# Optimization experiments

Hardware: AMD Instinct MI355X
Metric: run time of the kernel (lower is better)

The kernel has to match this reference:

```python
import jax, jax.numpy as jnp
import numpy as np

D_MODEL, D_INNER, D_STATE, DT_RANK, K = 768, 1536, 16, 48, 4
B, L = 2, 1024


def causal_depthwise_conv(x, w, b):
    # x: [B, L, D], w: [D, 1, K], b: [D]; torch pads K-1 both sides then slices [:L] -> causal left pad
    xt = x.transpose(0, 2, 1)  # [B, D, L]
    out = jax.lax.conv_general_dilated(
        xt, w, window_strides=(1,), padding=[(K - 1, 0)],
        dimension_numbers=('NCH', 'OIH', 'NCH'), feature_group_count=xt.shape[1])
    return out.transpose(0, 2, 1) + b


def ssm(xc, A_log, D, W_dt, dtW, dtb, W_B, W_C):
    # xc: [B, L, Din]
    A = -jnp.exp(A_log)                                   # [Din, N]
    dt_low = jnp.einsum('bld,rd->blr', xc, W_dt)          # [B, L, R]
    delta = jax.nn.softplus(jnp.einsum('blr,dr->bld', dt_low, dtW) + dtb)  # [B, L, Din]
    Bm = jnp.einsum('bld,nd->bln', xc, W_B)               # [B, L, N]
    Cm = jnp.einsum('bld,nd->bln', xc, W_C)               # [B, L, N]
    deltaA = jnp.exp(delta[..., None] * A)                # [B, L, Din, N]
    BX = (delta * xc)[..., None] * Bm[:, :, None, :]      # [B, L, Din, N]

    def combine(e1, e2):
        a1, b1 = e1
        a2, b2 = e2
        return a1 * a2, a2 * b1 + b2

    _, hs = jax.lax.associative_scan(combine, (deltaA, BX), axis=1)  # [B, L, Din, N]
    y = jnp.einsum('bldn,bln->bld', hs, Cm) + D * xc
    return y


def setup_inputs() -> dict:
    key = jax.random.key(0)
    ks = jax.random.split(key, 20)
    s = 0.02
    A_init = jnp.log(jnp.broadcast_to(jnp.arange(1, D_STATE + 1, dtype=jnp.float32), (D_INNER, D_STATE)))
    return {
        'x': jax.random.normal(ks[0], (B, L, D_MODEL), jnp.float32),
        'W_in_states': jax.random.normal(ks[1], (D_INNER, D_MODEL), jnp.float32) * s,
        'W_in_gates': jax.random.normal(ks[2], (D_INNER, D_MODEL), jnp.float32) * s,
        'conv_w': jax.random.normal(ks[3], (D_INNER, 1, K), jnp.float32) * 0.2,
        'conv_b': jax.random.normal(ks[4], (D_INNER,), jnp.float32) * 0.02,
        'conv_w_b': jax.random.normal(ks[5], (D_INNER, 1, K), jnp.float32) * 0.2,
        'conv_b_b': jax.random.normal(ks[6], (D_INNER,), jnp.float32) * 0.02,
        'W_dt': jax.random.normal(ks[7], (DT_RANK, D_INNER), jnp.float32) * s,
        'W_B': jax.random.normal(ks[8], (D_STATE, D_INNER), jnp.float32) * s,
        'W_C': jax.random.normal(ks[9], (D_STATE, D_INNER), jnp.float32) * s,
        'dtW': jax.random.normal(ks[10], (D_INNER, DT_RANK), jnp.float32) * s,
        'dtb': jax.random.normal(ks[11], (D_INNER,), jnp.float32) * 0.1,
        'A_log': A_init,
        'Dp': jnp.ones((D_INNER,), jnp.float32),
        'W_dt_b': jax.random.normal(ks[12], (DT_RANK, D_INNER), jnp.float32) * s,
        'W_B_b': jax.random.normal(ks[13], (D_STATE, D_INNER), jnp.float32) * s,
        'W_C_b': jax.random.normal(ks[14], (D_STATE, D_INNER), jnp.float32) * s,
        'dtW_b': jax.random.normal(ks[15], (D_INNER, DT_RANK), jnp.float32) * s,
        'dtb_b': jax.random.normal(ks[16], (D_INNER,), jnp.float32) * 0.1,
        'A_log_b': A_init,
        'Dp_b': jnp.ones((D_INNER,), jnp.float32),
        'W_out': jax.random.normal(ks[17], (D_MODEL, D_INNER), jnp.float32) * s,
    }


def reference(x, W_in_states, W_in_gates, conv_w, conv_b, conv_w_b, conv_b_b,
              W_dt, W_B, W_C, dtW, dtb, A_log, Dp,
              W_dt_b, W_B_b, W_C_b, dtW_b, dtb_b, A_log_b, Dp_b, W_out):
    xs = jnp.einsum('blm,dm->bld', x, W_in_states)  # [B, L, Din]
    z = jnp.einsum('blm,dm->bld', x, W_in_gates)    # [B, L, Din]
    # forward branch
    xc = jax.nn.silu(causal_depthwise_conv(xs, conv_w, conv_b))
    y = ssm(xc, A_log, Dp, W_dt, dtW, dtb, W_B, W_C)
    # backward branch: xz flipped along L, split -> reversed xs / reversed z
    xs_b = xs[:, ::-1]
    z_b = z[:, ::-1]
    xcb = jax.nn.silu(causal_depthwise_conv(xs_b, conv_w_b, conv_b_b))
    y_b = ssm(xcb, A_log_b, Dp_b, W_dt_b, dtW_b, dtb_b, W_B_b, W_C_b)
    # gating
    y = y * jax.nn.silu(z)
    y_b = y_b * jax.nn.silu(z_b)
    y = (y + y_b[:, ::-1]) * 0.5  # divide_output
    return jnp.einsum('bld,md->blm', y, W_out)
```

## Files before the change

### kernel.cpp

```cpp
#include <hip/hip_runtime.h>
#include <hip/hip_bf16.h>
#include <stdint.h>

#define DM 768
#define DI 1536
#define DSTATE 16
#define RNK 48
#define BB 2
#define LL 1024
#define ML (BB * LL)

#define NSEG 32
#define SEGL (LL / NSEG)

#define PROJ_NCHUNK 8
#define PROJ_KC (DI / PROJ_NCHUNK)

typedef unsigned short u16;
typedef __bf16 bf16x8 __attribute__((ext_vector_type(8)));
typedef float f32x4 __attribute__((ext_vector_type(4)));

struct __align__(8) u16x4_t { u16 x, y, z, w; };

__device__ __forceinline__ float b2f(u16 u) {
  union { uint32_t i; float f; } v; v.i = ((uint32_t)u) << 16; return v.f;
}
__device__ __forceinline__ u16 f2b(float f) {
  union { float f; uint32_t i; } v; v.f = f;
  uint32_t r = v.i + 0x7FFFu + ((v.i >> 16) & 1u);
  return (u16)(r >> 16);
}
__device__ __forceinline__ float silu_f(float x) { return x / (1.f + __expf(-x)); }
__device__ __forceinline__ float softplus_f(float s) {
  return fmaxf(s, 0.f) + __logf(1.f + __expf(-fabsf(s)));
}
__device__ __forceinline__ u16x4_t cvt4(float4 v) {
  u16x4_t o; o.x = f2b(v.x); o.y = f2b(v.y); o.z = f2b(v.z); o.w = f2b(v.w); return o;
}

__device__ __forceinline__ void gl16(const u16* g, u16* l) {
  __builtin_amdgcn_global_load_lds(
      (const __attribute__((address_space(1))) uint32_t*)g,
      (__attribute__((address_space(3))) uint32_t*)l, 16, 0, 0);
}

#define SEG_X    (ML * DM / 4)
#define SEG_W    (DI * DM / 4)
#define SEG_CAT  (128 * DI / 4)
#define SEG_DTW  (DI * 64 / 4)
__global__ __launch_bounds__(256) void convert_kernel(
    const float4* __restrict__ x, const float4* __restrict__ wis,
    const float4* __restrict__ wig, const float4* __restrict__ wout,
    const float* __restrict__ W_B, const float* __restrict__ W_C,
    const float* __restrict__ W_dt,
    const float* __restrict__ W_B_b, const float* __restrict__ W_C_b,
    const float* __restrict__ W_dt_b,
    const float* __restrict__ dtW, const float* __restrict__ dtW_b,
    u16x4_t* __restrict__ xb, u16x4_t* __restrict__ wisb,
    u16x4_t* __restrict__ wigb, u16x4_t* __restrict__ woutb,
    u16x4_t* __restrict__ wcf, u16x4_t* __restrict__ wcb,
    u16x4_t* __restrict__ dtwf, u16x4_t* __restrict__ dtwb)
{
  int idx = blockIdx.x * 256 + threadIdx.x;
  if (idx < SEG_X) { xb[idx] = cvt4(x[idx]); return; }
  idx -= SEG_X;
  if (idx < SEG_W) { wisb[idx] = cvt4(wis[idx]); return; }
  idx -= SEG_W;
  if (idx < SEG_W) { wigb[idx] = cvt4(wig[idx]); return; }
  idx -= SEG_W;
  if (idx < SEG_W) { woutb[idx] = cvt4(wout[idx]); return; }
  idx -= SEG_W;
  if (idx < 2 * SEG_CAT) {
    int dir = idx / SEG_CAT;
    int rem = idx % SEG_CAT;
    int row = rem / (DI / 4), k4 = rem % (DI / 4);
    const float* src = nullptr;
    if (row < 16)      src = (dir ? W_B_b  : W_B)  + (size_t)row * DI + k4 * 4;
    else if (row < 32) src = (dir ? W_C_b  : W_C)  + (size_t)(row - 16) * DI + k4 * 4;
    else if (row < 80) src = (dir ? W_dt_b : W_dt) + (size_t)(row - 32) * DI + k4 * 4;
    u16x4_t o;
    if (src) o = cvt4(*(const float4*)src);
    else { o.x = 0; o.y = 0; o.z = 0; o.w = 0; }
    (dir ? wcb : wcf)[rem] = o;
    return;
  }
  idx -= 2 * SEG_CAT;
  int dir = idx / SEG_DTW;
  int rem = idx % SEG_DTW;
  int d = rem / 16, r4 = rem % 16;
  const float* Dw = dir ? dtW_b : dtW;
  u16x4_t o;
  if (r4 < 12) o = cvt4(*(const float4*)(Dw + (size_t)d * RNK + r4 * 4));
  else { o.x = 0; o.y = 0; o.z = 0; o.w = 0; }
  (dir ? dtwb : dtwf)[rem] = o;
}

__global__ __launch_bounds__(256) void gemm_bt(
    const u16* __restrict__ A, const u16* __restrict__ B0,
    const u16* __restrict__ B1, int Nsplit,
    void* __restrict__ Cout, int M, int N, int K, int ldc, int epi)
{
  __shared__ alignas(16) u16 As[2][64 * 32];
  __shared__ alignas(16) u16 Bs[2][128 * 32];
  const int tid = threadIdx.x;
  const int wave = tid >> 6, lane = tid & 63;
  const int bm = blockIdx.y * 64;
  const int bn = blockIdx.x * 128;

  const u16* Bmat = B0;
  int ncol0 = bn;
  int epi_l = epi;
  if (B1 != nullptr && bn >= Nsplit) { Bmat = B1; ncol0 = bn - Nsplit; epi_l = 1; }

  const int c0 = tid, c1 = tid + 256;
  const u16* gA0 = A + (size_t)(bm + (c0 >> 2)) * K + (c0 & 3) * 8;
  const u16* gB0 = Bmat + (size_t)(ncol0 + (c0 >> 2)) * K + (c0 & 3) * 8;
  const u16* gB1 = Bmat + (size_t)(ncol0 + (c1 >> 2)) * K + (c1 & 3) * 8;

  const int wm = (wave & 1) * 32, wn = (wave >> 1) * 64;
  const int rl = lane & 15, q = lane >> 4;

  f32x4 acc[2][4];
#pragma unroll
  for (int i = 0; i < 2; ++i)
#pragma unroll
    for (int j = 0; j < 4; ++j) acc[i][j] = (f32x4){0.f, 0.f, 0.f, 0.f};

  auto stage = [&](int buf, int k0) {
    gl16(gA0 + k0, &As[buf][c0 * 8]);
    gl16(gB0 + k0, &Bs[buf][c0 * 8]);
    gl16(gB1 + k0, &Bs[buf][c1 * 8]);
  };

  stage(0, 0);
  __syncthreads();
  int cur = 0;
  for (int k0 = 0; k0 < K; k0 += 32) {
    const bool more = (k0 + 32 < K);
    if (more) stage(cur ^ 1, k0 + 32);

    const bf16x8* AsV = (const bf16x8*)As[cur];
    const bf16x8* BsV = (const bf16x8*)Bs[cur];
    bf16x8 af[2], bfv[4];
#pragma unroll
    for (int s = 0; s < 2; ++s)
      af[s] = AsV[(wm + s * 16 + rl) * 4 + q];
#pragma unroll
    for (int j = 0; j < 4; ++j)
      bfv[j] = BsV[(wn + j * 16 + rl) * 4 + q];
#pragma unroll
    for (int i = 0; i < 2; ++i)
#pragma unroll
      for (int j = 0; j < 4; ++j)
        acc[i][j] = __builtin_amdgcn_mfma_f32_16x16x32_bf16(af[i], bfv[j], acc[i][j], 0, 0, 0);

    if (more) {
      __syncthreads();
      cur ^= 1;
    }
  }

#pragma unroll
  for (int i = 0; i < 2; ++i) {
#pragma unroll
    for (int j = 0; j < 4; ++j) {
#pragma unroll
      for (int r = 0; r < 4; ++r) {
        int row = bm + wm + i * 16 + q * 4 + r;
        int col = bn + wn + j * 16 + rl;
        float v = acc[i][j][r];
        if (epi_l == 1) v = silu_f(v);
        ((u16*)Cout)[(size_t)row * ldc + col] = f2b(v);
      }
    }
  }
}

__global__ __launch_bounds__(256) void gemm_proj_sk(
    const u16* __restrict__ xcf, const u16* __restrict__ xcb,
    const u16* __restrict__ wcf, const u16* __restrict__ wcb,
    float* __restrict__ part)
{
  const int dir = blockIdx.z;
  const u16* A = dir ? xcb : xcf;
  const u16* B = dir ? wcb : wcf;
  const int kc = blockIdx.x;
  const int bm = blockIdx.y * 128;
  const int kbase = kc * PROJ_KC;

  __shared__ alignas(16) u16 As[128 * 32];
  __shared__ alignas(16) u16 Bs[128 * 32];
  const int tid = threadIdx.x;
  const int wave = tid >> 6, lane = tid & 63;
  const int c0 = tid, c1 = tid + 256;
  const u16* gA0 = A + (size_t)(bm + (c0 >> 2)) * DI + kbase + (c0 & 3) * 8;
  const u16* gA1 = A + (size_t)(bm + (c1 >> 2)) * DI + kbase + (c1 & 3) * 8;
  const u16* gB0 = B + (size_t)(c0 >> 2) * DI + kbase + (c0 & 3) * 8;
  const u16* gB1 = B + (size_t)(c1 >> 2) * DI + kbase + (c1 & 3) * 8;
  uint4* lA0 = (uint4*)&As[c0 * 8]; uint4* lA1 = (uint4*)&As[c1 * 8];
  uint4* lB0 = (uint4*)&Bs[c0 * 8]; uint4* lB1 = (uint4*)&Bs[c1 * 8];

  const int wm = (wave & 1) * 64, wn = (wave >> 1) * 64;
  const int rl = lane & 15, q = lane >> 4;

  f32x4 acc[4][4];
#pragma unroll
  for (int i = 0; i < 4; ++i)
#pragma unroll
    for (int j = 0; j < 4; ++j) acc[i][j] = (f32x4){0.f, 0.f, 0.f, 0.f};

  const bf16x8* AsV = (const bf16x8*)As;
  const bf16x8* BsV = (const bf16x8*)Bs;

  uint4 ra0 = *(const uint4*)(gA0);
  uint4 ra1 = *(const uint4*)(gA1);
  uint4 rb0 = *(const uint4*)(gB0);
  uint4 rb1 = *(const uint4*)(gB1);

  for (int k0 = 0; k0 < PROJ_KC; k0 += 32) {
    *lA0 = ra0; *lA1 = ra1; *lB0 = rb0; *lB1 = rb1;
    __syncthreads();
    if (k0 + 32 < PROJ_KC) {
      ra0 = *(const uint4*)(gA0 + k0 + 32);
      ra1 = *(const uint4*)(gA1 + k0 + 32);
      rb0 = *(const uint4*)(gB0 + k0 + 32);
      rb1 = *(const uint4*)(gB1 + k0 + 32);
    }
    bf16x8 af[4], bfv[4];
#pragma unroll
    for (int s = 0; s < 4; ++s) {
      af[s]  = AsV[(wm + s * 16 + rl) * 4 + q];
      bfv[s] = BsV[(wn + s * 16 + rl) * 4 + q];
    }
#pragma unroll
    for (int i = 0; i < 4; ++i)
#pragma unroll
      for (int j = 0; j < 4; ++j)
        acc[i][j] = __builtin_amdgcn_mfma_f32_16x16x32_bf16(af[i], bfv[j], acc[i][j], 0, 0, 0);
    __syncthreads();
  }

  float* pout = part + ((size_t)(dir * PROJ_NCHUNK + kc) * ML + bm) * 128;
#pragma unroll
  for (int i = 0; i < 4; ++i) {
#pragma unroll
    for (int j = 0; j < 4; ++j) {
#pragma unroll
      for (int r = 0; r < 4; ++r) {
        int row = wm + i * 16 + q * 4 + r;
        int col = wn + j * 16 + rl;
        if (col < 96)
          pout[(size_t)row * 128 + col] = acc[i][j][r];
      }
    }
  }
}

__global__ __launch_bounds__(256) void proj_reduce(
    const float* __restrict__ part,
    float* __restrict__ pf, float* __restrict__ pb,
    u16* __restrict__ dtlf, u16* __restrict__ dtlb)
{
  int idx = blockIdx.x * 256 + threadIdx.x;
  int col = idx % 96;
  int t = idx / 96;
  int row = t % ML;
  int dir = t / ML;
  const float* p = part + ((size_t)dir * PROJ_NCHUNK * ML + row) * 128 + col;
  float s = 0.f;
#pragma unroll
  for (int c = 0; c < PROJ_NCHUNK; ++c)
    s += p[(size_t)c * ML * 128];
  if (col < 32) (dir ? pb : pf)[(size_t)row * 32 + col] = s;
  else          (dir ? dtlb : dtlf)[(size_t)row * 64 + (col - 32)] = f2b(s);
}

__global__ __launch_bounds__(256) void gemm_delta(
    const u16* __restrict__ dtlf, const u16* __restrict__ dtlb,
    const u16* __restrict__ dtwf, const u16* __restrict__ dtwb,
    const float* __restrict__ dtb, const float* __restrict__ dtb_b,
    u16* __restrict__ df, u16* __restrict__ db)
{
  const int dir = blockIdx.z;
  const u16* A = dir ? dtlb : dtlf;
  const u16* Bw = dir ? dtwb : dtwf;
  const float* eb = dir ? dtb_b : dtb;
  u16* Cout = dir ? db : df;
  const int bm = blockIdx.y * 128;
  const int bn = blockIdx.x * 128;

  __shared__ alignas(16) u16 As[128 * 64];
  __shared__ alignas(16) u16 Bs[128 * 64];
  const int tid = threadIdx.x;
  const int wave = tid >> 6, lane = tid & 63;

#pragma unroll
  for (int i = 0; i < 4; ++i) {
    int c = tid + i * 256;
    gl16(A  + (size_t)(bm + (c >> 3)) * 64 + (c & 7) * 8, &As[c * 8]);
    gl16(Bw + (size_t)(bn + (c >> 3)) * 64 + (c & 7) * 8, &Bs[c * 8]);
  }
  __syncthreads();

  const int wm = (wave & 1) * 64, wn = (wave >> 1) * 64;
  const int rl = lane & 15, q = lane >> 4;

  f32x4 acc[4][4];
#pragma unroll
  for (int i = 0; i < 4; ++i)
#pragma unroll
    for (int j = 0; j < 4; ++j) acc[i][j] = (f32x4){0.f, 0.f, 0.f, 0.f};

#pragma unroll
  for (int kk = 0; kk < 2; ++kk) {
    bf16x8 af[4], bfv[4];
#pragma unroll
    for (int s = 0; s < 4; ++s) {
      af[s]  = *(const bf16x8*)&As[(wm + s * 16 + rl) * 64 + kk * 32 + q * 8];
      bfv[s] = *(const bf16x8*)&Bs[(wn + s * 16 + rl) * 64 + kk * 32 + q * 8];
    }
#pragma unroll
    for (int i = 0; i < 4; ++i)
#pragma unroll
      for (int j = 0; j < 4; ++j)
        acc[i][j] = __builtin_amdgcn_mfma_f32_16x16x32_bf16(af[i], bfv[j], acc[i][j], 0, 0, 0);
  }

#pragma unroll
  for (int i = 0; i < 4; ++i) {
#pragma unroll
    for (int j = 0; j < 4; ++j) {
#pragma unroll
      for (int r = 0; r < 4; ++r) {
        int row = bm + wm + i * 16 + q * 4 + r;
        int col = bn + wn + j * 16 + rl;
        Cout[(size_t)row * DI + col] = f2b(softplus_f(acc[i][j][r] + eb[col]));
      }
    }
  }
}

__global__ __launch_bounds__(256) void gemm_out64(
    const u16* __restrict__ A, const u16* __restrict__ Bw,
    float* __restrict__ out)
{
  __shared__ alignas(16) u16 As[64 * 72];
  __shared__ alignas(16) u16 Bs[64 * 72];
  const int tid = threadIdx.x;
  const int wave = tid >> 6, lane = tid & 63;
  const int bm = blockIdx.y * 64;
  const int bn = blockIdx.x * 64;

  const int c0 = tid, c1 = tid + 256;
  const u16* gA0 = A + (size_t)(bm + (c0 >> 3)) * DI + (c0 & 7) * 8;
  const u16* gA1 = A + (size_t)(bm + (c1 >> 3)) * DI + (c1 & 7) * 8;
  const u16* gB0 = Bw + (size_t)(bn + (c0 >> 3)) * DI + (c0 & 7) * 8;
  const u16* gB1 = Bw + (size_t)(bn + (c1 >> 3)) * DI + (c1 & 7) * 8;
  uint4* lA0 = (uint4*)&As[(c0 >> 3) * 72 + (c0 & 7) * 8];
  uint4* lA1 = (uint4*)&As[(c1 >> 3) * 72 + (c1 & 7) * 8];
  uint4* lB0 = (uint4*)&Bs[(c0 >> 3) * 72 + (c0 & 7) * 8];
  uint4* lB1 = (uint4*)&Bs[(c1 >> 3) * 72 + (c1 & 7) * 8];

  const int rl = lane & 15, q = lane >> 4;

  f32x4 acc[4];
#pragma unroll
  for (int s = 0; s < 4; ++s) acc[s] = (f32x4){0.f, 0.f, 0.f, 0.f};

  uint4 ra0 = *(const uint4*)gA0, ra1 = *(const uint4*)gA1;
  uint4 rb0 = *(const uint4*)gB0, rb1 = *(const uint4*)gB1;

  for (int k0 = 0; k0 < DI; k0 += 64) {
    *lA0 = ra0; *lA1 = ra1; *lB0 = rb0; *lB1 = rb1;
    __syncthreads();
    if (k0 + 64 < DI) {
      ra0 = *(const uint4*)(gA0 + k0 + 64);
      ra1 = *(const uint4*)(gA1 + k0 + 64);
      rb0 = *(const uint4*)(gB0 + k0 + 64);
      rb1 = *(const uint4*)(gB1 + k0 + 64);
    }
    bf16x8 bf[2], af;
#pragma unroll
    for (int c = 0; c < 2; ++c)
      bf[c] = *(const bf16x8*)&Bs[(wave * 16 + rl) * 72 + c * 32 + q * 8];
#pragma unroll
    for (int s = 0; s < 4; ++s) {
#pragma unroll
      for (int c = 0; c < 2; ++c) {
        af = *(const bf16x8*)&As[(s * 16 + rl) * 72 + c * 32 + q * 8];
        acc[s] = __builtin_amdgcn_mfma_f32_16x16x32_bf16(af, bf[c], acc[s], 0, 0, 0);
      }
    }
    __syncthreads();
  }

#pragma unroll
  for (int s = 0; s < 4; ++s) {
#pragma unroll
    for (int r = 0; r < 4; ++r) {
      int row = bm + s * 16 + q * 4 + r;
      int col = bn + wave * 16 + rl;
      out[(size_t)row * DM + col] = acc[s][r];
    }
  }
}

__global__ void conv_kernel(
    const u16* __restrict__ xsg,
    const float* __restrict__ cw, const float* __restrict__ cb,
    const float* __restrict__ cwb, const float* __restrict__ cbb,
    u16* __restrict__ xc, u16* __restrict__ xcb)
{
  int idx = blockIdx.x * 256 + threadIdx.x;
  int d = idx % DI;
  int row = idx / DI;
  int l = row % LL, b = row / LL;
  const u16* base = xsg + (size_t)b * LL * 3072 + d;

  float4 wf = *(const float4*)(cw + d * 4);
  float4 wb = *(const float4*)(cwb + d * 4);
  float wfk[4] = {wf.x, wf.y, wf.z, wf.w};
  float wbk[4] = {wb.x, wb.y, wb.z, wb.w};

  float accf = cb[d];
  float accb = cbb[d];
#pragma unroll
  for (int k = 0; k < 4; ++k) {
    int ls = l - 3 + k;
    if (ls >= 0) {
      accf += wfk[k] * b2f(base[(size_t)ls * 3072]);
      accb += wbk[k] * b2f(base[(size_t)(LL - 1 - ls) * 3072]);
    }
  }
  xc[idx]  = f2b(silu_f(accf));
  xcb[idx] = f2b(silu_f(accb));
}

__global__ __launch_bounds__(256) void scan_sum(
    const u16* __restrict__ df, const u16* __restrict__ db,
    const u16* __restrict__ xcf, const u16* __restrict__ xcb,
    const float* __restrict__ pf, const float* __restrict__ pb,
    const float* __restrict__ A_log, const float* __restrict__ A_log_b,
    float* __restrict__ sdl, float* __restrict__ bs)
{
  const int dir = blockIdx.z / NSEG, seg = blockIdx.z % NSEG;
  const u16* delta = dir ? db : df;
  const u16* xc = dir ? xcb : xcf;
  const float* proj = dir ? pb : pf;
  const float* Al = dir ? A_log_b : A_log;
  const int b = blockIdx.y;
  const int d = blockIdx.x * 256 + threadIdx.x;
  const int l0 = seg * SEGL;

  __shared__ float Bsh[SEGL][16];
  for (int i = threadIdx.x; i < SEGL * 16; i += 256) {
    int l = i >> 4, n = i & 15;
    Bsh[l][n] = proj[((size_t)b * LL + l0 + l) * 32 + n];
  }
  __syncthreads();

  float An[16];
#pragma unroll
  for (int n = 0; n < 16; ++n) An[n] = -__expf(Al[d * 16 + n]);

  float h[16];
#pragma unroll
  for (int n = 0; n < 16; ++n) h[n] = 0.f;
  float S = 0.f;

  const u16* dbase = delta + ((size_t)b * LL + l0) * DI + d;
  const u16* xbase = xc + ((size_t)b * LL + l0) * DI + d;

  for (int g = 0; g < SEGL; g += 4) {
    float dl4[4], dx4[4];
#pragma unroll
    for (int j = 0; j < 4; ++j) {
      float dv = b2f(dbase[(size_t)(g + j) * DI]);
      float xv = b2f(xbase[(size_t)(g + j) * DI]);
      dl4[j] = dv; dx4[j] = dv * xv;
    }
#pragma unroll
    for (int j = 0; j < 4; ++j) {
      S += dl4[j];
#pragma unroll
      for (int n = 0; n < 16; ++n)
        h[n] = __expf(dl4[j] * An[n]) * h[n] + dx4[j] * Bsh[g + j][n];
    }
  }

  size_t base = (((size_t)dir * BB + b) * NSEG + seg) * DI + d;
  sdl[base] = S;
#pragma unroll
  for (int n = 0; n < 16; ++n) bs[base * 16 + n] = h[n];
}

__global__ __launch_bounds__(256) void scan_carry(
    const float* __restrict__ A_log, const float* __restrict__ A_log_b,
    const float* __restrict__ sdl, float* __restrict__ bs)
{
  int idx = blockIdx.x * 256 + threadIdx.x;
  int n = idx & 15;
  int t = idx >> 4;
  int d = t % DI;
  int b = (t / DI) % BB;
  int dir = t / (DI * BB);
  const float* Al = dir ? A_log_b : A_log;
  float An = -__expf(Al[d * 16 + n]);
  float h = 0.f;
  for (int s = 0; s < NSEG; ++s) {
    size_t base = (((size_t)dir * BB + b) * NSEG + s) * DI + d;
    float S = sdl[base];
    float bv = bs[base * 16 + n];
    bs[base * 16 + n] = h;
    h = __expf(S * An) * h + bv;
  }
}

__global__ __launch_bounds__(512) void scan_apply2(
    const u16* __restrict__ df, const u16* __restrict__ db,
    const u16* __restrict__ xcf, const u16* __restrict__ xcb,
    const float* __restrict__ pf, const float* __restrict__ pb,
    const float* __restrict__ A_log, const float* __restrict__ A_log_b,
    const float* __restrict__ Dp, const float* __restrict__ Dp_b,
    const float* __restrict__ bs, const u16* __restrict__ xsg,
    u16* __restrict__ yc)
{
  const int s = blockIdx.z;
  const int b = blockIdx.y;
  const int tid = threadIdx.x;
  const int half = tid >> 8;
  const int td = tid & 255;
  const int d = blockIdx.x * 256 + td;

  __shared__ float BCsh[2][SEGL][32];
  __shared__ u16 ysh[2][SEGL][256];

  const int seg = half ? (NSEG - 1 - s) : s;
  const int l0 = seg * SEGL;
  const float* proj = half ? pb : pf;
  const float* Al   = half ? A_log_b : A_log;
  const float* Dpp  = half ? Dp_b : Dp;
  const u16* delta  = half ? db : df;
  const u16* xc     = half ? xcb : xcf;

  for (int i = td; i < SEGL * 32; i += 256) {
    int l = i >> 5, j = i & 31;
    BCsh[half][l][j] = proj[((size_t)b * LL + l0 + l) * 32 + j];
  }
  __syncthreads();

  float An[16];
#pragma unroll
  for (int n = 0; n < 16; ++n) An[n] = -__expf(Al[d * 16 + n]);
  const float Dv = Dpp[d];

  float h[16];
  size_t cbase = (((size_t)half * BB + b) * NSEG + seg) * DI + d;
#pragma unroll
  for (int n = 0; n < 16; ++n) h[n] = bs[cbase * 16 + n];

  const u16* dbase = delta + ((size_t)b * LL + l0) * DI + d;
  const u16* xbase = xc + ((size_t)b * LL + l0) * DI + d;

  for (int g = 0; g < SEGL; g += 4) {
    float dl4[4], xv4[4];
#pragma unroll
    for (int j = 0; j < 4; ++j) {
      dl4[j] = b2f(dbase[(size_t)(g + j) * DI]);
      xv4[j] = b2f(xbase[(size_t)(g + j) * DI]);
    }
#pragma unroll
    for (int j = 0; j < 4; ++j) {
      float dx = dl4[j] * xv4[j];
      float yv = 0.f;
#pragma unroll
      for (int n = 0; n < 16; ++n) {
        h[n] = __expf(dl4[j] * An[n]) * h[n] + dx * BCsh[half][g + j][n];
        yv += h[n] * BCsh[half][g + j][16 + n];
      }
      ysh[half][g + j][td] = f2b(yv + Dv * xv4[j]);
    }
  }
  __syncthreads();

  for (int i = tid; i < SEGL * 256; i += 512) {
    int lrow = i >> 8, dd = i & 255;
    int l = s * SEGL + lrow;
    int dg = blockIdx.x * 256 + dd;
    float gate = b2f(xsg[((size_t)b * LL + l) * 3072 + DI + dg]);
    float out = 0.5f * (b2f(ysh[0][lrow][dd]) +
                        b2f(ysh[1][SEGL - 1 - lrow][dd])) * gate;
    yc[((size_t)b * LL + l) * DI + dg] = f2b(out);
  }
}

extern "C" void kernel_launch(void* const* d_in, const int* in_sizes, int n_in,
                              void* d_out, int out_size, void* d_ws, size_t ws_size,
                              hipStream_t stream)
{
  const float* x       = (const float*)d_in[0];
  const float* Wis     = (const float*)d_in[1];
  const float* Wig     = (const float*)d_in[2];
  const float* conv_w  = (const float*)d_in[3];
  const float* conv_b  = (const float*)d_in[4];
  const float* conv_wb = (const float*)d_in[5];
  const float* conv_bb = (const float*)d_in[6];
  const float* W_dt    = (const float*)d_in[7];
  const float* W_B     = (const float*)d_in[8];
  const float* W_C     = (const float*)d_in[9];
  const float* dtW     = (const float*)d_in[10];
  const float* dtb     = (const float*)d_in[11];
  const float* A_log   = (const float*)d_in[12];
  const float* Dp      = (const float*)d_in[13];
  const float* W_dt_b  = (const float*)d_in[14];
  const float* W_B_b   = (const float*)d_in[15];
  const float* W_C_b   = (const float*)d_in[16];
  const float* dtW_b   = (const float*)d_in[17];
  const float* dtb_b   = (const float*)d_in[18];
  const float* A_log_b = (const float*)d_in[19];
  const float* Dp_b    = (const float*)d_in[20];
  const float* W_out   = (const float*)d_in[21];

  char* ws = (char*)d_ws;
  size_t off = 0;
  auto alloc = [&](size_t bytes) -> char* {
    char* p = ws + off; off += (bytes + 255) & ~(size_t)255; return p;
  };
  u16*   xb    = (u16*)alloc((size_t)ML * DM * 2);
  u16*   wisb  = (u16*)alloc((size_t)DI * DM * 2);
  u16*   wigb  = (u16*)alloc((size_t)DI * DM * 2);
  u16*   woutb = (u16*)alloc((size_t)DM * DI * 2);
  u16*   xsg = (u16*)alloc((size_t)ML * 3072 * 2);
  u16*   xc  = (u16*)alloc((size_t)ML * DI * 2);
  u16*   xcb = (u16*)alloc((size_t)ML * DI * 2);
  u16*   wcf = (u16*)alloc((size_t)128 * DI * 2);
  u16*   wcb = (u16*)alloc((size_t)128 * DI * 2);
  u16*   dtwf = (u16*)alloc((size_t)DI * 64 * 2);
  u16*   dtwb = (u16*)alloc((size_t)DI * 64 * 2);
  float* pf  = (float*)alloc((size_t)ML * 32 * 4);
  float* pb  = (float*)alloc((size_t)ML * 32 * 4);
  u16*   dtlf = (u16*)alloc((size_t)ML * 64 * 2);
  u16*   dtlb = (u16*)alloc((size_t)ML * 64 * 2);
  u16*   df  = (u16*)alloc((size_t)ML * DI * 2);
  u16*   db  = (u16*)alloc((size_t)ML * DI * 2);
  u16*   yc  = (u16*)alloc((size_t)ML * DI * 2);
  float* sdl = (float*)alloc((size_t)2 * BB * NSEG * DI * 4);
  float* bs  = (float*)alloc((size_t)2 * BB * NSEG * DI * 16 * 4);
  float* part = (float*)alloc((size_t)2 * PROJ_NCHUNK * ML * 128 * 4);

  const int conv_total = SEG_X + 3 * SEG_W + 2 * SEG_CAT + 2 * SEG_DTW;
  convert_kernel<<<(conv_total + 255) / 256, 256, 0, stream>>>(
      (const float4*)x, (const float4*)Wis, (const float4*)Wig, (const float4*)W_out,
      W_B, W_C, W_dt, W_B_b, W_C_b, W_dt_b, dtW, dtW_b,
      (u16x4_t*)xb, (u16x4_t*)wisb, (u16x4_t*)wigb, (u16x4_t*)woutb,
      (u16x4_t*)wcf, (u16x4_t*)wcb, (u16x4_t*)dtwf, (u16x4_t*)dtwb);

  gemm_bt<<<dim3(3072 / 128, ML / 64, 1), 256, 0, stream>>>(
      xb, wisb, wigb, DI, xsg, ML, 3072, DM, 3072, 0);

  conv_kernel<<<(ML * DI) / 256, 256, 0, stream>>>(
      xsg, conv_w, conv_b, conv_wb, conv_bb, xc, xcb);

  gemm_proj_sk<<<dim3(PROJ_NCHUNK, ML / 128, 2), 256, 0, stream>>>(
      xc, xcb, wcf, wcb, part);
  proj_reduce<<<(2 * ML * 96) / 256, 256, 0, stream>>>(
      part, pf, pb, dtlf, dtlb);

  gemm_delta<<<dim3(DI / 128, ML / 128, 2), 256, 0, stream>>>(
      dtlf, dtlb, dtwf, dtwb, dtb, dtb_b, df, db);

  scan_sum<<<dim3(DI / 256, BB, 2 * NSEG), 256, 0, stream>>>(
      df, db, xc, xcb, pf, pb, A_log, A_log_b, sdl, bs);
  scan_carry<<<(2 * BB * DI * 16) / 256, 256, 0, stream>>>(
      A_log, A_log_b, sdl, bs);
  scan_apply2<<<dim3(DI / 256, BB, NSEG), 512, 0, stream>>>(
      df, db, xc, xcb, pf, pb, A_log, A_log_b, Dp, Dp_b, bs, xsg, yc);

  gemm_out64<<<dim3(DM / 64, ML / 64, 1), 256, 0, stream>>>(
      yc, woutb, (float*)d_out);
}
```

Measured before the change: 256.4 us.

## Store delta and conv output channel-major so scans load contiguous time vectors

The delta GEMM swaps its operands so it writes delta in [D, B*L] layout, and the conv kernel now computes 8 consecutive timesteps per thread and also writes transposed copies of xc/xcb. The scan kernels then read 8 bf16 timesteps per 16-byte load instead of strided per-timestep scalar loads. This is meant to cut memory transactions in the scan phase. In exchange it adds extra transposed buffers and 16-byte-strided writes in conv, plus transposed stores in gemm_delta that may coalesce less well.

```diff
diff --git a/kernel.cpp b/kernel.cpp
--- a/kernel.cpp
+++ b/kernel.cpp
@@ -282,8 +282,8 @@
     u16* __restrict__ df, u16* __restrict__ db)
 {
   const int dir = blockIdx.z;
-  const u16* A = dir ? dtlb : dtlf;
-  const u16* Bw = dir ? dtwb : dtwf;
+  const u16* Aw = dir ? dtwb : dtwf;
+  const u16* Bl = dir ? dtlb : dtlf;
   const float* eb = dir ? dtb_b : dtb;
   u16* Cout = dir ? db : df;
   const int bm = blockIdx.y * 128;
@@ -297,8 +297,8 @@
 #pragma unroll
   for (int i = 0; i < 4; ++i) {
     int c = tid + i * 256;
-    gl16(A  + (size_t)(bm + (c >> 3)) * 64 + (c & 7) * 8, &As[c * 8]);
-    gl16(Bw + (size_t)(bn + (c >> 3)) * 64 + (c & 7) * 8, &Bs[c * 8]);
+    gl16(Aw + (size_t)(bm + (c >> 3)) * 64 + (c & 7) * 8, &As[c * 8]);
+    gl16(Bl + (size_t)(bn + (c >> 3)) * 64 + (c & 7) * 8, &Bs[c * 8]);
   }
   __syncthreads();
 
@@ -334,7 +334,7 @@
       for (int r = 0; r < 4; ++r) {
         int row = bm + wm + i * 16 + q * 4 + r;
         int col = bn + wn + j * 16 + rl;
-        Cout[(size_t)row * DI + col] = f2b(softplus_f(acc[i][j][r] + eb[col]));
+        Cout[(size_t)row * ML + col] = f2b(softplus_f(acc[i][j][r] + eb[row]));
       }
     }
   }
@@ -405,35 +405,53 @@
   }
 }
 
-__global__ void conv_kernel(
+__global__ __launch_bounds__(256) void conv_kernel(
     const u16* __restrict__ xsg,
     const float* __restrict__ cw, const float* __restrict__ cb,
     const float* __restrict__ cwb, const float* __restrict__ cbb,
-    u16* __restrict__ xc, u16* __restrict__ xcb)
-{
-  int idx = blockIdx.x * 256 + threadIdx.x;
-  int d = idx % DI;
-  int row = idx / DI;
-  int l = row % LL, b = row / LL;
+    u16* __restrict__ xc, u16* __restrict__ xcb,
+    u16* __restrict__ xct, u16* __restrict__ xcbt)
+{
+  int g = blockIdx.x * 256 + threadIdx.x;
+  int d = g % DI;
+  int lg = g / DI;
+  int b = lg >> 7;
+  int l0 = (lg & 127) * 8;
   const u16* base = xsg + (size_t)b * LL * 3072 + d;
 
   float4 wf = *(const float4*)(cw + d * 4);
   float4 wb = *(const float4*)(cwb + d * 4);
   float wfk[4] = {wf.x, wf.y, wf.z, wf.w};
   float wbk[4] = {wb.x, wb.y, wb.z, wb.w};
-
-  float accf = cb[d];
-  float accb = cbb[d];
-#pragma unroll
-  for (int k = 0; k < 4; ++k) {
-    int ls = l - 3 + k;
+  const float cbf = cb[d], cbbv = cbb[d];
+
+  float f[11], r[11];
+#pragma unroll
+  for (int j = 0; j < 11; ++j) {
+    int ls = l0 - 3 + j;
     if (ls >= 0) {
-      accf += wfk[k] * b2f(base[(size_t)ls * 3072]);
-      accb += wbk[k] * b2f(base[(size_t)(LL - 1 - ls) * 3072]);
-    }
-  }
-  xc[idx]  = f2b(silu_f(accf));
-  xcb[idx] = f2b(silu_f(accb));
+      f[j] = b2f(base[(size_t)ls * 3072]);
+      r[j] = b2f(base[(size_t)(LL - 1 - ls) * 3072]);
+    } else { f[j] = 0.f; r[j] = 0.f; }
+  }
+
+  u16 otf[8], otb[8];
+#pragma unroll
+  for (int t = 0; t < 8; ++t) {
+    float accf = cbf, accb = cbbv;
+#pragma unroll
+    for (int k = 0; k < 4; ++k) {
+      accf += wfk[k] * f[t + k];
+      accb += wbk[k] * r[t + k];
+    }
+    u16 vf = f2b(silu_f(accf));
+    u16 vb = f2b(silu_f(accb));
+    xc [((size_t)(b * LL + l0 + t)) * DI + d] = vf;
+    xcb[((size_t)(b * LL + l0 + t)) * DI + d] = vb;
+    otf[t] = vf; otb[t] = vb;
+  }
+  *(uint4*)&xct [(size_t)d * ML + b * LL + l0] = *(const uint4*)otf;
+  *(uint4*)&xcbt[(size_t)d * ML + b * LL + l0] = *(const uint4*)otb;
 }
 
 __global__ __launch_bounds__(256) void scan_sum(
@@ -468,23 +486,23 @@
   for (int n = 0; n < 16; ++n) h[n] = 0.f;
   float S = 0.f;
 
-  const u16* dbase = delta + ((size_t)b * LL + l0) * DI + d;
-  const u16* xbase = xc + ((size_t)b * LL + l0) * DI + d;
-
-  for (int g = 0; g < SEGL; g += 4) {
-    float dl4[4], dx4[4];
-#pragma unroll
-    for (int j = 0; j < 4; ++j) {
-      float dv = b2f(dbase[(size_t)(g + j) * DI]);
-      float xv = b2f(xbase[(size_t)(g + j) * DI]);
-      dl4[j] = dv; dx4[j] = dv * xv;
-    }
-#pragma unroll
-    for (int j = 0; j < 4; ++j) {
-      S += dl4[j];
+  const u16* dbase = delta + (size_t)d * ML + b * LL + l0;
+  const u16* xbase = xc + (size_t)d * ML + b * LL + l0;
+
+  for (int g = 0; g < SEGL; g += 8) {
+    uint4 dv = *(const uint4*)(dbase + g);
+    uint4 xv = *(const uint4*)(xbase + g);
+    uint32_t dw[4] = {dv.x, dv.y, dv.z, dv.w};
+    uint32_t xw[4] = {xv.x, xv.y, xv.z, xv.w};
+#pragma unroll
+    for (int jj = 0; jj < 8; ++jj) {
+      float dl = b2f((u16)(dw[jj >> 1] >> ((jj & 1) * 16)));
+      float xvv = b2f((u16)(xw[jj >> 1] >> ((jj & 1) * 16)));
+      float dx = dl * xvv;
+      S += dl;
 #pragma unroll
       for (int n = 0; n < 16; ++n)
-        h[n] = __expf(dl4[j] * An[n]) * h[n] + dx4[j] * Bsh[g + j][n];
+        h[n] = __expf(dl * An[n]) * h[n] + dx * Bsh[g + jj][n];
     }
   }
 
@@ -559,26 +577,26 @@
 #pragma unroll
   for (int n = 0; n < 16; ++n) h[n] = bs[cbase * 16 + n];
 
-  const u16* dbase = delta + ((size_t)b * LL + l0) * DI + d;
-  const u16* xbase = xc + ((size_t)b * LL + l0) * DI + d;
-
-  for (int g = 0; g < SEGL; g += 4) {
-    float dl4[4], xv4[4];
-#pragma unroll
-    for (int j = 0; j < 4; ++j) {
-      dl4[j] = b2f(dbase[(size_t)(g + j) * DI]);
-      xv4[j] = b2f(xbase[(size_t)(g + j) * DI]);
-    }
-#pragma unroll
-    for (int j = 0; j < 4; ++j) {
-      float dx = dl4[j] * xv4[j];
+  const u16* dbase = delta + (size_t)d * ML + b * LL + l0;
+  const u16* xbase = xc + (size_t)d * ML + b * LL + l0;
+
+  for (int g = 0; g < SEGL; g += 8) {
+    uint4 dv = *(const uint4*)(dbase + g);
+    uint4 xv = *(const uint4*)(xbase + g);
+    uint32_t dw[4] = {dv.x, dv.y, dv.z, dv.w};
+    uint32_t xw[4] = {xv.x, xv.y, xv.z, xv.w};
+#pragma unroll
+    for (int jj = 0; jj < 8; ++jj) {
+      float dl = b2f((u16)(dw[jj >> 1] >> ((jj & 1) * 16)));
+      float xvv = b2f((u16)(xw[jj >> 1] >> ((jj & 1) * 16)));
+      float dx = dl * xvv;
       float yv = 0.f;
 #pragma unroll
       for (int n = 0; n < 16; ++n) {
-        h[n] = __expf(dl4[j] * An[n]) * h[n] + dx * BCsh[half][g + j][n];
-        yv += h[n] * BCsh[half][g + j][16 + n];
+        h[n] = __expf(dl * An[n]) * h[n] + dx * BCsh[half][g + jj][n];
+        yv += h[n] * BCsh[half][g + jj][16 + n];
       }
-      ysh[half][g + j][td] = f2b(yv + Dv * xv4[j]);
+      ysh[half][g + jj][td] = f2b(yv + Dv * xvv);
     }
   }
   __syncthreads();
@@ -633,6 +651,8 @@
   u16*   xsg = (u16*)alloc((size_t)ML * 3072 * 2);
   u16*   xc  = (u16*)alloc((size_t)ML * DI * 2);
   u16*   xcb = (u16*)alloc((size_t)ML * DI * 2);
+  u16*   xct  = (u16*)alloc((size_t)ML * DI * 2);
+  u16*   xcbt = (u16*)alloc((size_t)ML * DI * 2);
   u16*   wcf = (u16*)alloc((size_t)128 * DI * 2);
   u16*   wcb = (u16*)alloc((size_t)128 * DI * 2);
   u16*   dtwf = (u16*)alloc((size_t)DI * 64 * 2);
@@ -658,23 +678,23 @@
   gemm_bt<<<dim3(3072 / 128, ML / 64, 1), 256, 0, stream>>>(
       xb, wisb, wigb, DI, xsg, ML, 3072, DM, 3072, 0);
 
-  conv_kernel<<<(ML * DI) / 256, 256, 0, stream>>>(
-      xsg, conv_w, conv_b, conv_wb, conv_bb, xc, xcb);
+  conv_kernel<<<(ML / 8 * DI) / 256, 256, 0, stream>>>(
+      xsg, conv_w, conv_b, conv_wb, conv_bb, xc, xcb, xct, xcbt);
 
   gemm_proj_sk<<<dim3(PROJ_NCHUNK, ML / 128, 2), 256, 0, stream>>>(
       xc, xcb, wcf, wcb, part);
   proj_reduce<<<(2 * ML * 96) / 256, 256, 0, stream>>>(
       part, pf, pb, dtlf, dtlb);
 
-  gemm_delta<<<dim3(DI / 128, ML / 128, 2), 256, 0, stream>>>(
+  gemm_delta<<<dim3(ML / 128, DI / 128, 2), 256, 0, stream>>>(
       dtlf, dtlb, dtwf, dtwb, dtb, dtb_b, df, db);
 
   scan_sum<<<dim3(DI / 256, BB, 2 * NSEG), 256, 0, stream>>>(
-      df, db, xc, xcb, pf, pb, A_log, A_log_b, sdl, bs);
+      df, db, xct, xcbt, pf, pb, A_log, A_log_b, sdl, bs);
   scan_carry<<<(2 * BB * DI * 16) / 256, 256, 0, stream>>>(
       A_log, A_log_b, sdl, bs);
   scan_apply2<<<dim3(DI / 256, BB, NSEG), 512, 0, stream>>>(
-      df, db, xc, xcb, pf, pb, A_log, A_log_b, Dp, Dp_b, bs, xsg, yc);
+      df, db, xct, xcbt, pf, pb, A_log, A_log_b, Dp, Dp_b, bs, xsg, yc);
 
   gemm_out64<<<dim3(DM / 64, ML / 64, 1), 256, 0, stream>>>(
       yc, woutb, (float*)d_out);
```

Result: no change. 261.1 us (+1.8%).
